# Kernel tuning notes

Measured on AMD Instinct MI355X. Metric: run time of the kernel, lower is better.

The kernel has to match this reference:

```python
import jax, jax.numpy as jnp
import numpy as np

L_LAYERS, D, H, FF_MUL = 4, 512, 8, 4
VOCAB, SEQ, MEM, CMEM, RATIO = 32000, 1024, 1024, 256, 4
DH = D // H


def _ln(x, g, b):
    mu = jnp.mean(x, -1, keepdims=True)
    var = jnp.mean((x - mu) ** 2, -1, keepdims=True)
    return (x - mu) / jnp.sqrt(var + 1e-5) * g + b


def _heads(x):
    b, n, _ = x.shape
    return x.reshape(b, n, H, -1).transpose(0, 2, 1, 3)  # [b,h,n,dh]


def _shift(x):
    # relative-position shift trick, x: [b,h,i,j] -> [b,h,i,j]
    b, h, i, j = x.shape
    x = jnp.concatenate([x, jnp.zeros((b, h, i, i), x.dtype)], -1)
    l = i + j - 1
    x = x.reshape(b, h, i * (i + j))
    pad = (-x.shape[-1]) % l
    x = jnp.pad(x, ((0, 0), (0, 0), (0, pad))).reshape(b, h, -1, l)
    return x[:, :, :i, i - 1:]


def _conv(x, w, b):
    # x: [B,L,D], w: [D_out, D_in, RATIO] (OIH), stride=RATIO
    y = jax.lax.conv_general_dilated(x.transpose(0, 2, 1), w, (RATIO,), 'VALID',
                                     dimension_numbers=('NCH', 'OIH', 'NCH'))
    return y.transpose(0, 2, 1) + b


def _full_attn(q, k, v):
    dots = jnp.einsum('bhid,bhjd->bhij', q, k) * (q.shape[-1] ** -0.5)
    return jnp.einsum('bhij,bhjd->bhid', jax.nn.softmax(dots, -1), v)


def setup_inputs() -> dict:
    key = jax.random.key(0)
    ks = jax.random.split(key, 24)
    s = 0.02
    return {
        'seq': jax.random.randint(ks[0], (4, SEQ), 0, VOCAB),
        'mask': jnp.ones((4, SEQ), dtype=bool),
        'mems': jax.random.normal(ks[1], (L_LAYERS, 4, MEM, D)) * s,
        'cmems': jax.random.normal(ks[2], (L_LAYERS, 4, CMEM, D)) * s,
        'pos_emb': jax.random.normal(ks[3], (H, CMEM + MEM + SEQ, DH)) * s,
        'embed': jax.random.normal(ks[4], (VOCAB, D)) * s,
        'ln1_g': jnp.ones((L_LAYERS, D)), 'ln1_b': jnp.zeros((L_LAYERS, D)),
        'Wq': jax.random.normal(ks[5], (L_LAYERS, D, D)) * s,
        'Wkv': jax.random.normal(ks[6], (L_LAYERS, D, 2 * D)) * s,
        'Wo': jax.random.normal(ks[7], (L_LAYERS, D, D)) * s,
        'bo': jnp.zeros((L_LAYERS, D)),
        'conv_w': jax.random.normal(ks[8], (L_LAYERS, D, D, RATIO)) * s,
        'conv_b': jnp.zeros((L_LAYERS, D)),
        'ln2_g': jnp.ones((L_LAYERS, D)), 'ln2_b': jnp.zeros((L_LAYERS, D)),
        'W1': jax.random.normal(ks[9], (L_LAYERS, D, FF_MUL * D)) * s,
        'b1': jnp.zeros((L_LAYERS, FF_MUL * D)),
        'W2': jax.random.normal(ks[10], (L_LAYERS, FF_MUL * D, D)) * s,
        'b2': jnp.zeros((L_LAYERS, D)),
    }


def _forward(seq, mask, mems, cmems, pos_emb, embed, ln1_g, ln1_b, Wq, Wkv, Wo, bo,
             conv_w, conv_b, ln2_g, ln2_b, W1, b1, W2, b2):
    scale = DH ** -0.5
    x = embed[seq]  # [b,t,d]
    maskb = mask.astype(bool)
    new_mems, new_cmems = [], []
    aux_total = jnp.zeros((), x.dtype)
    w_acc = 0.0
    for l in range(L_LAYERS):
        mem, cmem = mems[l], cmems[l]
        xn = _ln(x, ln1_g[l], ln1_b[l])
        q = _heads(xn @ Wq[l])
        kv_in = jnp.concatenate([cmem, mem, xn], 1)  # [b,kv_len,d]
        kv_len = kv_in.shape[1]
        k, v = jnp.split(kv_in @ Wkv[l], 2, -1)
        k, v = _heads(k), _heads(v)
        dots = jnp.einsum('bhid,bhjd->bhij', q, k) * scale
        pe = pos_emb[:, -kv_len:]
        dots = dots + _shift(jnp.einsum('bhid,hjd->bhij', q, pe) * scale)
        m2 = maskb[:, None, :, None] & maskb[:, None, None, :]  # [b,1,t,t]
        m2 = jnp.pad(m2, ((0, 0), (0, 0), (0, 0), (kv_len - SEQ, 0)), constant_values=True)
        dots = jnp.where(m2, dots, -jnp.finfo(dots.dtype).max)
        attn = jax.nn.softmax(dots, -1)
        w_acc = w_acc + jnp.mean(jax.lax.stop_gradient(attn), axis=(0, 1))
        out = jnp.einsum('bhij,bhjd->bhid', attn, v)
        out = out.transpose(0, 2, 1, 3).reshape(x.shape[0], SEQ, D)
        x = x + out @ Wo[l] + bo[l]
        # FIFO memory update (queue normed x, evict oldest)
        queue = jnp.concatenate([mem, xn], 1)
        old_mem, new_mem = queue[:, :-MEM], queue[:, -MEM:]
        pad_amt = old_mem.shape[1] % RATIO
        if pad_amt:
            old_mem = jnp.pad(old_mem, ((0, 0), (pad_amt, 0), (0, 0)))
        comp = _conv(old_mem, conv_w[l], conv_b[l])
        new_cmem = jnp.concatenate([cmem, comp], 1)[:, -CMEM:]
        new_mems.append(new_mem)
        new_cmems.append(new_cmem)
        # reconstruction (attention-reconstruction) aux loss
        old_mem_d = jax.lax.stop_gradient(old_mem)
        comp2 = _conv(old_mem_d, conv_w[l], conv_b[l])
        ck, cv = jnp.split(comp2 @ jax.lax.stop_gradient(Wkv[l]), 2, -1)
        ck, cv = _heads(ck), _heads(cv)
        start = kv_len - min(mem.shape[1], MEM) - SEQ
        ok = jax.lax.stop_gradient(k[:, :, start:kv_len - SEQ])
        ov = jax.lax.stop_gradient(v[:, :, start:kv_len - SEQ])
        qd = jax.lax.stop_gradient(q)
        aux_total = aux_total + jnp.mean((_full_attn(qd, ok, ov) - _full_attn(qd, ck, cv)) ** 2)
        # feed-forward block (PreNorm + Residual), exact GELU like torch nn.GELU
        xn2 = _ln(x, ln2_g[l], ln2_b[l])
        x = x + jax.nn.gelu(xn2 @ W1[l] + b1[l], approximate=False) @ W2[l] + b2[l]
    return (x, jnp.stack(new_mems), jnp.stack(new_cmems),
            aux_total / L_LAYERS, w_acc / L_LAYERS)


def reference(seq, mask, mems, cmems, pos_emb, embed, ln1_g, ln1_b, Wq, Wkv, Wo, bo,
              conv_w, conv_b, ln2_g, ln2_b, W1, b1, W2, b2):
    return _forward(seq, mask, mems, cmems, pos_emb, embed, ln1_g, ln1_b, Wq, Wkv, Wo, bo,
                    conv_w, conv_b, ln2_g, ln2_b, W1, b1, W2, b2)
```

## Files before the change

### kernel.cpp

```cpp
#include <hip/hip_runtime.h>
#include <hip/hip_bf16.h>


typedef __hip_bfloat16 bf16;
typedef short s16x8 __attribute__((ext_vector_type(8)));
typedef float f32x4 __attribute__((ext_vector_type(4)));

__device__ __forceinline__ f32x4 mfma16(s16x8 a, s16x8 b, f32x4 c) {
  return __builtin_amdgcn_mfma_f32_16x16x32_bf16(a, b, c, 0, 0, 0);
}

typedef __attribute__((address_space(1))) const void gvoid;
typedef __attribute__((address_space(3))) void lvoid;
__device__ __forceinline__ void gll16(const void* g, void* l) {
  __builtin_amdgcn_global_load_lds((gvoid*)g, (lvoid*)l, 16, 0, 0);
}

__device__ __forceinline__ float b2f(unsigned short u) {
  return __uint_as_float(((unsigned)u) << 16);
}
__device__ __forceinline__ unsigned short f2bb(float f) {
  bf16 h = __float2bfloat16(f);
  return *reinterpret_cast<unsigned short*>(&h);
}
__device__ __forceinline__ float ldf(const float* p) { return *p; }
__device__ __forceinline__ float ldf(const bf16* p) { return __bfloat162float(*p); }
__device__ __forceinline__ float4 ld4(const float* p) { return *(const float4*)p; }
__device__ __forceinline__ float4 ld4(const bf16* p) {
  const ushort4 u = *(const ushort4*)p;
  return make_float4(b2f(u.x), b2f(u.y), b2f(u.z), b2f(u.w));
}
__device__ __forceinline__ void st4(float* p, float4 r) { *(float4*)p = r; }
__device__ __forceinline__ void st4(bf16* p, float4 r) {
  *(ushort4*)p = make_ushort4(f2bb(r.x), f2bb(r.y), f2bb(r.z), f2bb(r.w));
}
__device__ __forceinline__ void stf(float* p, float v) { *p = v; }
__device__ __forceinline__ void stf(bf16* p, float v) { *p = __float2bfloat16(v); }

__global__ void probe_k(const void* ln1g, unsigned* flag) {
  if (threadIdx.x == 0) {
    const unsigned short u = *(const unsigned short*)ln1g;
    *flag = (u == 0x3F80u) ? 1u : 0u;
  }
}

template <int BM, int AMODE, bool ADD, bool BIAS, bool GELU, typename TC>
__global__ __launch_bounds__(256) void mgemm_k(
    const bf16* __restrict__ A, const int lda, const bf16* __restrict__ Bt,
    TC* __restrict__ C, const int ldc, const float* __restrict__ bias,
    const int K) {
  constexpr int NF = (BM == 128) ? 4 : 2;
  __shared__ bf16 As[BM * 64];
  __shared__ bf16 Bs[128 * 64];
  const int t = threadIdx.x, w = t >> 6, lane = t & 63;
  const int g = lane >> 4, li = lane & 15;
  const int m0 = blockIdx.y * BM, n0 = blockIdx.x << 7;
  const int wrow = (BM == 128) ? ((w >> 1) << 6) : 0;
  const int wcol = (BM == 128) ? ((w & 1) << 6) : (w << 5);
  f32x4 acc[4][NF];
#pragma unroll
  for (int mf = 0; mf < 4; mf++)
#pragma unroll
    for (int nf = 0; nf < NF; nf++)
#pragma unroll
      for (int e = 0; e < 4; e++) acc[mf][nf][e] = 0.f;
  constexpr int ACH = BM / 32;
  const int srow = lane >> 3, s8 = lane & 7;
  for (int k0 = 0; k0 < K; k0 += 64) {
    __syncthreads();
#pragma unroll
    for (int it = 0; it < ACH; it++) {
      const int chunk = w * ACH + it;
      const int row = (chunk << 3) + srow;
      const int k8 = s8 ^ (row & 7);
      const bf16* src;
      if constexpr (AMODE == 0) {
        src = A + (size_t)(m0 + row) * lda + k0 + (k8 << 3);
      } else if constexpr (AMODE == 1) {
        const int m = m0 + row;
        src = A + ((size_t)((m >> 8) * 2304 + 256) << 9) + (m & 255) * 2048 +
              k0 + (k8 << 3);
      } else {
        const int m = m0 + row;
        src = A + ((size_t)((m >> 10) * 2304 + 1280 + (m & 1023)) << 9) + k0 +
              (k8 << 3);
      }
      gll16(src, As + (chunk << 9));
    }
#pragma unroll
    for (int it = 0; it < 4; it++) {
      const int chunk = (w << 2) + it;
      const int row = (chunk << 3) + srow;
      const int k8 = s8 ^ (row & 7);
      gll16(Bt + (size_t)(n0 + row) * K + k0 + (k8 << 3), Bs + (chunk << 9));
    }
    __syncthreads();
#pragma unroll
    for (int ks = 0; ks < 2; ks++) {
      s16x8 af[4];
#pragma unroll
      for (int mf = 0; mf < 4; mf++) {
        const int row = wrow + (mf << 4) + li;
        af[mf] = *reinterpret_cast<const s16x8*>(
            As + (row << 6) + ((((ks << 2) + g) ^ (row & 7)) << 3));
      }
#pragma unroll
      for (int nf = 0; nf < NF; nf++) {
        const int col = wcol + (nf << 4) + li;
        const s16x8 bfr = *reinterpret_cast<const s16x8*>(
            Bs + (col << 6) + ((((ks << 2) + g) ^ (col & 7)) << 3));
#pragma unroll
        for (int mf = 0; mf < 4; mf++)
          acc[mf][nf] = mfma16(af[mf], bfr, acc[mf][nf]);
      }
    }
  }
#pragma unroll
  for (int mf = 0; mf < 4; mf++)
#pragma unroll
    for (int nf = 0; nf < NF; nf++) {
      const int n = n0 + wcol + (nf << 4) + li;
      const float bv = BIAS ? bias[n] : 0.f;
#pragma unroll
      for (int r = 0; r < 4; r++) {
        const int m = m0 + wrow + (mf << 4) + (g << 2) + r;
        float v = acc[mf][nf][r] + bv;
        if constexpr (GELU) v = 0.5f * v * (1.0f + erff(v * 0.70710678118f));
        TC* cp = C + (size_t)m * ldc + n;
        if constexpr (ADD)
          *cp += v;
        else
          stf(cp, v);
      }
    }
}

template <bool REL, bool DIFF, typename TO>
__global__ __launch_bounds__(256) void flash_k(
    const bf16* __restrict__ q, const bf16* __restrict__ kbase,
    const bf16* __restrict__ vbase, const int kvlen, const int ldkv,
    const int bstride, const bf16* __restrict__ pe, float2* __restrict__ ml,
    TO* __restrict__ outp, const float* __restrict__ prior,
    float* __restrict__ auxsum) {
  __shared__ short k_s[4096];
  __shared__ short v_s[4096];
  __shared__ short p_s[4096];
  __shared__ short pe_s[REL ? 8192 : 8];
  __shared__ float t_s[REL ? 5376 : 4];
  __shared__ float red_s[4];
  const int t = threadIdx.x, w = t >> 6, lane = t & 63;
  const int g = lane >> 4, li = lane & 15;
  const int i0 = blockIdx.x << 6, h = blockIdx.y, b = blockIdx.z;
  const bf16* qp =
      q + (size_t)(b * 1024 + i0 + (w << 4) + li) * 512 + (h << 6) + (g << 3);
  const s16x8 qf0 = *reinterpret_cast<const s16x8*>(qp);
  const s16x8 qf1 = *reinterpret_cast<const s16x8*>(qp + 32);
  const bf16* kpb = kbase + (size_t)b * bstride + (h << 6);
  const bf16* vpb = vbase + (size_t)b * bstride + (h << 6);
  const bf16* peh = REL ? pe + (size_t)h * 147456 : nullptr;
  float mreg[4] = {-1e30f, -1e30f, -1e30f, -1e30f};
  float lreg[4] = {0.f, 0.f, 0.f, 0.f};
  f32x4 o[4];
#pragma unroll
  for (int nt = 0; nt < 4; nt++)
#pragma unroll
    for (int e = 0; e < 4; e++) o[nt][e] = 0.f;

  for (int j0 = 0; j0 < kvlen; j0 += 64) {
    const int ub0 = j0 - i0 + 960;
    const bool doT = REL && (ub0 < 2304);
    __syncthreads();
    {
      const int r2 = t >> 3, c8 = t & 7;
#pragma unroll
      for (int it = 0; it < 2; it++) {
        const int row = (it << 5) + r2;
        const size_t gof = (size_t)(j0 + row) * ldkv + (c8 << 3);
        const s16x8 kk = *reinterpret_cast<const s16x8*>(kpb + gof);
        *reinterpret_cast<s16x8*>(
            k_s + (((row << 6) + (c8 << 3)) ^ ((row & 7) << 3))) = kk;
        const s16x8 vv = *reinterpret_cast<const s16x8*>(vpb + gof);
#pragma unroll
        for (int e = 0; e < 8; e++) {
          const int d = (c8 << 3) + e;
          v_s[((d << 6) + row) ^ (((c8 ^ e) & 7) << 3)] = vv[e];
        }
      }
      if (doT) {
#pragma unroll
        for (int it = 0; it < 4; it++) {
          const int idx = (it << 8) + t;
          const int row = idx >> 3, pc8 = idx & 7;
          const int u = ub0 + row;
          s16x8 pv = {0, 0, 0, 0, 0, 0, 0, 0};
          if (u < 2304)
            pv = *reinterpret_cast<const s16x8*>(peh + ((size_t)u << 6) + (pc8 << 3));
          *reinterpret_cast<s16x8*>(
              pe_s + (((row << 6) + (pc8 << 3)) ^ ((row & 7) << 3))) = pv;
        }
      }
    }
    __syncthreads();
    f32x4 s[4];
#pragma unroll
    for (int nt = 0; nt < 4; nt++) {
#pragma unroll
      for (int e = 0; e < 4; e++) s[nt][e] = 0.f;
      const int rb = (((nt << 4) + li) << 6) + (g << 3);
      const int sw = (li & 7) << 3;
      const s16x8 kb0 = *reinterpret_cast<const s16x8*>(k_s + (rb ^ sw));
      const s16x8 kb1 = *reinterpret_cast<const s16x8*>(k_s + ((rb + 32) ^ sw));
      s[nt] = mfma16(qf0, kb0, s[nt]);
      s[nt] = mfma16(qf1, kb1, s[nt]);
    }
    if (doT) {
      float* tw = t_s + w * 1344;
      const int urb = 48 - (w << 4);
#pragma unroll
      for (int ut = 0; ut < 5; ut++) {
        f32x4 tt;
#pragma unroll
        for (int e = 0; e < 4; e++) tt[e] = 0.f;
        const int prb = ((urb + (ut << 4) + li) << 6) + (g << 3);
        const int sw = (li & 7) << 3;
        const s16x8 pb0 = *reinterpret_cast<const s16x8*>(pe_s + (prb ^ sw));
        const s16x8 pb1 = *reinterpret_cast<const s16x8*>(pe_s + ((prb + 32) ^ sw));
        tt = mfma16(qf0, pb0, tt);
        tt = mfma16(qf1, pb1, tt);
#pragma unroll
        for (int r = 0; r < 4; r++) tw[((g << 2) + r) * 84 + (ut << 4) + li] = tt[r];
      }
#pragma unroll
      for (int nt = 0; nt < 4; nt++)
#pragma unroll
        for (int r = 0; r < 4; r++)
          s[nt][r] += tw[((g << 2) + r) * 83 + (nt << 4) + li + 15];
    }
#pragma unroll
    for (int nt = 0; nt < 4; nt++)
#pragma unroll
      for (int e = 0; e < 4; e++) s[nt][e] *= 0.125f;
    float pr[4][4];
#pragma unroll
    for (int r = 0; r < 4; r++) {
      float tm = fmaxf(fmaxf(s[0][r], s[1][r]), fmaxf(s[2][r], s[3][r]));
#pragma unroll
      for (int off = 1; off < 16; off <<= 1) tm = fmaxf(tm, __shfl_xor(tm, off));
      const float mn = fmaxf(mreg[r], tm);
      const float al = __expf(mreg[r] - mn);
      mreg[r] = mn;
      float te = 0.f;
#pragma unroll
      for (int nt = 0; nt < 4; nt++) {
        pr[nt][r] = __expf(s[nt][r] - mn);
        te += pr[nt][r];
      }
#pragma unroll
      for (int off = 1; off < 16; off <<= 1) te += __shfl_xor(te, off);
      lreg[r] = lreg[r] * al + te;
#pragma unroll
      for (int nt = 0; nt < 4; nt++) o[nt][r] *= al;
    }
    short* pw = p_s + (w << 10);
#pragma unroll
    for (int nt = 0; nt < 4; nt++)
#pragma unroll
      for (int r = 0; r < 4; r++) {
        const int il = (g << 2) + r;
        pw[((il << 6) + (nt << 4) + li) ^ ((il & 7) << 3)] = (short)f2bb(pr[nt][r]);
      }
#pragma unroll
    for (int ks = 0; ks < 2; ks++) {
      const s16x8 pa = *reinterpret_cast<const s16x8*>(
          pw + (((li << 6) + (ks << 5) + (g << 3)) ^ ((li & 7) << 3)));
#pragma unroll
      for (int nt = 0; nt < 4; nt++) {
        const int d = (nt << 4) + li;
        const s16x8 vb = *reinterpret_cast<const s16x8*>(
            v_s + (((d << 6) + (ks << 5) + (g << 3)) ^ ((((d >> 3) ^ (d & 7)) & 7) << 3)));
        o[nt] = mfma16(pa, vb, o[nt]);
      }
    }
  }
  float rl[4];
#pragma unroll
  for (int r = 0; r < 4; r++) rl[r] = 1.0f / lreg[r];
  if constexpr (REL) {
    if (li == 0) {
#pragma unroll
      for (int r = 0; r < 4; r++)
        ml[(size_t)((b << 3) + h) * 1024 + i0 + (w << 4) + (g << 2) + r] =
            make_float2(mreg[r], lreg[r]);
    }
  }
  if constexpr (!DIFF) {
#pragma unroll
    for (int nt = 0; nt < 4; nt++)
#pragma unroll
      for (int r = 0; r < 4; r++) {
        const size_t adr = (size_t)(b * 1024 + i0 + (w << 4) + (g << 2) + r) * 512 +
                           (h << 6) + (nt << 4) + li;
        stf(outp + adr, o[nt][r] * rl[r]);
      }
  } else {
    float sq = 0.f;
#pragma unroll
    for (int nt = 0; nt < 4; nt++)
#pragma unroll
      for (int r = 0; r < 4; r++) {
        const size_t adr = (size_t)(b * 1024 + i0 + (w << 4) + (g << 2) + r) * 512 +
                           (h << 6) + (nt << 4) + li;
        const float dv = o[nt][r] * rl[r] - prior[adr];
        sq = fmaf(dv, dv, sq);
      }
#pragma unroll
    for (int off = 1; off < 64; off <<= 1) sq += __shfl_xor(sq, off);
    if (lane == 0) red_s[w] = sq;
    __syncthreads();
    if (t == 0) atomicAdd(auxsum, red_s[0] + red_s[1] + red_s[2] + red_s[3]);
  }
}

__global__ __launch_bounds__(256) void wacc_k(const bf16* __restrict__ q,
                                              const bf16* __restrict__ kv,
                                              const bf16* __restrict__ pe,
                                              const float2* __restrict__ ml,
                                              float* __restrict__ w_acc) {
  __shared__ short k_s[4096];
  __shared__ short pe_s[8192];
  __shared__ float t_s[5376];
  __shared__ float2 ml_s[64];
  const int t = threadIdx.x, w = t >> 6, lane = t & 63;
  const int g = lane >> 4, li = lane & 15;
  const int i0 = blockIdx.x << 6, j0 = blockIdx.y << 6;
  const int ub0 = j0 - i0 + 960;
  const bool doT = (ub0 < 2304);
  f32x4 acc[4];
#pragma unroll
  for (int nt = 0; nt < 4; nt++)
#pragma unroll
    for (int e = 0; e < 4; e++) acc[nt][e] = 0.f;
  for (int h = 0; h < 8; h++) {
    __syncthreads();
    if (doT) {
      const bf16* peh = pe + (size_t)h * 147456;
#pragma unroll
      for (int it = 0; it < 4; it++) {
        const int idx = (it << 8) + t;
        const int row = idx >> 3, pc8 = idx & 7;
        const int u = ub0 + row;
        s16x8 pv = {0, 0, 0, 0, 0, 0, 0, 0};
        if (u < 2304)
          pv = *reinterpret_cast<const s16x8*>(peh + ((size_t)u << 6) + (pc8 << 3));
        *reinterpret_cast<s16x8*>(
            pe_s + (((row << 6) + (pc8 << 3)) ^ ((row & 7) << 3))) = pv;
      }
    }
    for (int b = 0; b < 4; b++) {
      __syncthreads();
      {
        const int r2 = t >> 3, c8 = t & 7;
        const bf16* kpb = kv + (size_t)b * 2359296 + (h << 6);
#pragma unroll
        for (int it = 0; it < 2; it++) {
          const int row = (it << 5) + r2;
          const s16x8 kk = *reinterpret_cast<const s16x8*>(
              kpb + (size_t)(j0 + row) * 1024 + (c8 << 3));
          *reinterpret_cast<s16x8*>(
              k_s + (((row << 6) + (c8 << 3)) ^ ((row & 7) << 3))) = kk;
        }
        if (t < 64) {
          float2 v = ml[(size_t)((b << 3) + h) * 1024 + i0 + t];
          v.y = 1.0f / v.y;
          ml_s[t] = v;
        }
      }
      __syncthreads();
      const bf16* qp =
          q + (size_t)(b * 1024 + i0 + (w << 4) + li) * 512 + (h << 6) + (g << 3);
      const s16x8 qf0 = *reinterpret_cast<const s16x8*>(qp);
      const s16x8 qf1 = *reinterpret_cast<const s16x8*>(qp + 32);
      f32x4 s[4];
#pragma unroll
      for (int nt = 0; nt < 4; nt++) {
#pragma unroll
        for (int e = 0; e < 4; e++) s[nt][e] = 0.f;
        const int rb = (((nt << 4) + li) << 6) + (g << 3);
        const int sw = (li & 7) << 3;
        const s16x8 kb0 = *reinterpret_cast<const s16x8*>(k_s + (rb ^ sw));
        const s16x8 kb1 = *reinterpret_cast<const s16x8*>(k_s + ((rb + 32) ^ sw));
        s[nt] = mfma16(qf0, kb0, s[nt]);
        s[nt] = mfma16(qf1, kb1, s[nt]);
      }
      if (doT) {
        float* tw = t_s + w * 1344;
        const int urb = 48 - (w << 4);
#pragma unroll
        for (int ut = 0; ut < 5; ut++) {
          f32x4 tt;
#pragma unroll
          for (int e = 0; e < 4; e++) tt[e] = 0.f;
          const int prb = ((urb + (ut << 4) + li) << 6) + (g << 3);
          const int sw = (li & 7) << 3;
          const s16x8 pb0 = *reinterpret_cast<const s16x8*>(pe_s + (prb ^ sw));
          const s16x8 pb1 = *reinterpret_cast<const s16x8*>(pe_s + ((prb + 32) ^ sw));
          tt = mfma16(qf0, pb0, tt);
          tt = mfma16(qf1, pb1, tt);
#pragma unroll
          for (int r = 0; r < 4; r++)
            tw[((g << 2) + r) * 84 + (ut << 4) + li] = tt[r];
        }
#pragma unroll
        for (int nt = 0; nt < 4; nt++)
#pragma unroll
          for (int r = 0; r < 4; r++)
            s[nt][r] += tw[((g << 2) + r) * 83 + (nt << 4) + li + 15];
      }
#pragma unroll
      for (int nt = 0; nt < 4; nt++)
#pragma unroll
        for (int r = 0; r < 4; r++) {
          const float sv = s[nt][r] * 0.125f;
          const float2 st = ml_s[(w << 4) + (g << 2) + r];
          acc[nt][r] += __expf(sv - st.x) * st.y;
        }
    }
  }
#pragma unroll
  for (int nt = 0; nt < 4; nt++)
#pragma unroll
    for (int r = 0; r < 4; r++) {
      float* wp = w_acc + (size_t)(i0 + (w << 4) + (g << 2) + r) * 2304 + j0 +
                  (nt << 4) + li;
      *wp += acc[nt][r];
    }
}

template <typename TIN>
__global__ __launch_bounds__(256) void wtr_k(
    const TIN* __restrict__ Wq, const TIN* __restrict__ Wkv,
    const TIN* __restrict__ Wo, const TIN* __restrict__ W1,
    const TIN* __restrict__ W2, bf16* __restrict__ WT,
    const unsigned* flag, unsigned want) {
  if (*flag != want) return;
  __shared__ bf16 tile[64][65];
  int bx = blockIdx.x;
  const TIN* W;
  bf16* dst;
  int N, K;
  if (bx < 64) {
    W = Wq; dst = WT; N = 512; K = 512;
  } else if (bx < 192) {
    W = Wkv; dst = WT + 262144; N = 1024; K = 512; bx -= 64;
  } else if (bx < 256) {
    W = Wo; dst = WT + 786432; N = 512; K = 512; bx -= 192;
  } else if (bx < 512) {
    W = W1; dst = WT + 1048576; N = 2048; K = 512; bx -= 256;
  } else {
    W = W2; dst = WT + 2097152; N = 512; K = 2048; bx -= 512;
  }
  const int tn = N >> 6;
  const int kt = bx / tn, nt = bx - kt * tn;
  const int k0 = kt << 6, n0 = nt << 6;
  const int t = threadIdx.x;
#pragma unroll
  for (int i = 0; i < 16; i++) {
    const int idx = (i << 8) + t;
    const int kr = idx >> 6, nc = idx & 63;
    tile[kr][nc] = __float2bfloat16(ldf(W + (size_t)(k0 + kr) * N + n0 + nc));
  }
  __syncthreads();
#pragma unroll
  for (int i = 0; i < 16; i++) {
    const int idx = (i << 8) + t;
    const int nr = idx >> 6, kc = idx & 63;
    dst[(size_t)(n0 + nr) * K + k0 + kc] = tile[kc][nr];
  }
}

template <typename TIN>
__global__ void wcp_k(const TIN* __restrict__ cw, bf16* __restrict__ WcT,
                      const unsigned* flag, unsigned want) {
  if (*flag != want) return;
  const int id = blockIdx.x * 256 + threadIdx.x;
  const int o = id >> 11, p = id & 2047;
  const int r = p >> 9, i = p & 511;
  WcT[id] = __float2bfloat16(ldf(cw + ((size_t)o << 11) + (i << 2) + r));
}

template <typename TIN>
__global__ void kvb_k(const TIN* __restrict__ cmem, const TIN* __restrict__ mem,
                      bf16* __restrict__ kvin, const unsigned* flag, unsigned want) {
  if (*flag != want) return;
  const int id = blockIdx.x * 256 + threadIdx.x;
  const int row = id >> 7, c4 = (id & 127) << 2;
  const int b = row / 1280, j = row - b * 1280;
  const TIN* src = (j < 256) ? cmem + (((size_t)(b * 256 + j)) << 9) + c4
                             : mem + (((size_t)(b * 1024 + j - 256)) << 9) + c4;
  st4(kvin + (((size_t)(b * 2304 + j)) << 9) + c4, ld4(src));
}

template <typename TIN>
__global__ void bcvt_k(const TIN* __restrict__ bo, const TIN* __restrict__ cb,
                       const TIN* __restrict__ b1, const TIN* __restrict__ b2,
                       float* __restrict__ bws, const unsigned* flag, unsigned want) {
  if (*flag != want) return;
  const int id = blockIdx.x * 256 + threadIdx.x;
  const int l = id / 3584, r = id - l * 3584;
  float v;
  if (r < 512) v = ldf(bo + l * 512 + r);
  else if (r < 1024) v = ldf(cb + l * 512 + r - 512);
  else if (r < 3072) v = ldf(b1 + l * 2048 + r - 1024);
  else v = ldf(b2 + l * 512 + r - 3072);
  bws[id] = v;
}

template <typename TIN, typename TY>
__global__ __launch_bounds__(256) void ln_k(const float* __restrict__ x,
                                            const TIN* __restrict__ g,
                                            const TIN* __restrict__ bta,
                                            TY* __restrict__ y, bf16* kvx,
                                            const unsigned* flag, unsigned want) {
  if (*flag != want) return;
  const int w = threadIdx.x >> 6, lane = threadIdx.x & 63;
  const size_t row = (size_t)blockIdx.x * 4 + w;
  const float* xr = x + row * 512;
  float v[8], s = 0, ss = 0;
#pragma unroll
  for (int i = 0; i < 8; i++) {
    v[i] = xr[lane + (i << 6)];
    s += v[i];
    ss = fmaf(v[i], v[i], ss);
  }
#pragma unroll
  for (int off = 1; off < 64; off <<= 1) {
    s += __shfl_xor(s, off);
    ss += __shfl_xor(ss, off);
  }
  const float mu = s * (1.0f / 512.0f);
  const float var = ss * (1.0f / 512.0f) - mu * mu;
  const float inv = rsqrtf(var + 1e-5f);
  bf16* k2 = kvx ? kvx + (((row >> 10) * 2304 + 1280 + (row & 1023)) << 9) : nullptr;
#pragma unroll
  for (int i = 0; i < 8; i++) {
    const int c = lane + (i << 6);
    const float val = (v[i] - mu) * inv * ldf(g + c) + ldf(bta + c);
    stf(y + row * 512 + c, val);
    if (k2) k2[c] = __float2bfloat16(val);
  }
}

template <typename TIN>
__global__ void embed_k(const int* __restrict__ seq, const TIN* __restrict__ emb,
                        float* __restrict__ x, const unsigned* flag, unsigned want) {
  if (*flag != want) return;
  const int row = blockIdx.x;
  const int tok = seq[row];
  const TIN* e = emb + (size_t)tok * 512;
  float* xr = x + (size_t)row * 512;
  for (int c = threadIdx.x; c < 512; c += 256) xr[c] = ldf(e + c);
}

template <typename TIN>
__global__ void cvtpe_k(const TIN* __restrict__ pe, bf16* __restrict__ peb,
                        const unsigned* flag, unsigned want) {
  if (*flag != want) return;
  const int i = blockIdx.x * 256 + threadIdx.x;
  peb[i] = __float2bfloat16(ldf(pe + i));
}

__global__ void zero_k(float* __restrict__ p, int n) {
  for (int i = blockIdx.x * 256 + threadIdx.x; i < n; i += gridDim.x * 256) p[i] = 0.0f;
}

template <typename TOUT>
__global__ void cpy_k(const bf16* __restrict__ s, TOUT* __restrict__ d, int n,
                      const unsigned* flag, unsigned want) {
  if (*flag != want) return;
  for (int i = blockIdx.x * 256 + threadIdx.x; i < n; i += gridDim.x * 256)
    stf(d + i, ldf(s + i));
}

template <typename TOUT>
__global__ void f2bs_k(const float* __restrict__ s, TOUT* __restrict__ d, float sc,
                       int n, const unsigned* flag, unsigned want) {
  if (*flag != want) return;
  for (int i = blockIdx.x * 256 + threadIdx.x; i < n; i += gridDim.x * 256)
    stf(d + i, s[i] * sc);
}

template <typename TOUT>
__global__ void fin_aux_k(const float* __restrict__ acc, TOUT* __restrict__ d,
                          const unsigned* flag, unsigned want) {
  if (*flag != want) return;
  if (threadIdx.x == 0) stf(d, acc[0] * (1.0f / 8388608.0f));
}

extern "C" void kernel_launch(void* const* d_in, const int* in_sizes, int n_in,
                              void* d_out, int out_size, void* d_ws, size_t ws_size,
                              hipStream_t stream) {
  typedef const bf16 CB;
  typedef const float CF;
  const int* seq = (const int*)d_in[0];
  CB *mems_b = (CB*)d_in[2], *cmems_b = (CB*)d_in[3], *pe_b = (CB*)d_in[4],
     *emb_b = (CB*)d_in[5], *l1g_b = (CB*)d_in[6], *l1b_b = (CB*)d_in[7],
     *Wq_b = (CB*)d_in[8], *Wkv_b = (CB*)d_in[9], *Wo_b = (CB*)d_in[10],
     *bo_b = (CB*)d_in[11], *cw_b = (CB*)d_in[12], *cb_b = (CB*)d_in[13],
     *l2g_b = (CB*)d_in[14], *l2b_b = (CB*)d_in[15], *W1_b = (CB*)d_in[16],
     *b1_b = (CB*)d_in[17], *W2_b = (CB*)d_in[18], *b2_b = (CB*)d_in[19];
  CF *mems_f = (CF*)d_in[2], *cmems_f = (CF*)d_in[3], *pe_f = (CF*)d_in[4],
     *emb_f = (CF*)d_in[5], *l1g_f = (CF*)d_in[6], *l1b_f = (CF*)d_in[7],
     *Wq_f = (CF*)d_in[8], *Wkv_f = (CF*)d_in[9], *Wo_f = (CF*)d_in[10],
     *bo_f = (CF*)d_in[11], *cw_f = (CF*)d_in[12], *cb_f = (CF*)d_in[13],
     *l2g_f = (CF*)d_in[14], *l2b_f = (CF*)d_in[15], *W1_f = (CF*)d_in[16],
     *b1_f = (CF*)d_in[17], *W2_f = (CF*)d_in[18], *b2_f = (CF*)d_in[19];
  bf16* outb = (bf16*)d_out;
  float* outf = (float*)d_out;

  float* ws = (float*)d_ws;
  float* x = ws;
  bf16* q = (bf16*)(ws + 2097152);
  bf16* kv = (bf16*)(ws + 3145728);
  bf16* mid = (bf16*)(ws + 3145728);
  float* region = ws + 7864320;
  bf16* attn_o = (bf16*)region;
  float* aux1 = region;
  bf16* xn2 = (bf16*)region;
  bf16* ckcv = (bf16*)(ws + 9961472);
  float* w_acc = ws + 10485760;
  bf16* cmp_ws = (bf16*)(ws + 12845056);
  float2* ml = (float2*)(ws + 13369344);
  float* auxsum = ws + 13434880;
  unsigned* flag = (unsigned*)(ws + 13434881);
  bf16* pe_w = (bf16*)(ws + 13434884);
  float* bias_ws = ws + 14024708;
  bf16* kvin = (bf16*)(ws + 14039044);
  bf16* WT = (bf16*)(ws + 16398340);

  probe_k<<<1, 64, 0, stream>>>(d_in[6], flag);
  zero_k<<<2048, 256, 0, stream>>>(w_acc, 2359296);
  zero_k<<<1, 256, 0, stream>>>(auxsum, 1);
  embed_k<bf16><<<4096, 256, 0, stream>>>(seq, emb_b, x, flag, 1);
  embed_k<float><<<4096, 256, 0, stream>>>(seq, emb_f, x, flag, 0);
  cvtpe_k<bf16><<<4608, 256, 0, stream>>>(pe_b, pe_w, flag, 1);
  cvtpe_k<float><<<4608, 256, 0, stream>>>(pe_f, pe_w, flag, 0);
  bcvt_k<bf16><<<56, 256, 0, stream>>>(bo_b, cb_b, b1_b, b2_b, bias_ws, flag, 1);
  bcvt_k<float><<<56, 256, 0, stream>>>(bo_f, cb_f, b1_f, b2_f, bias_ws, flag, 0);

  for (int l = 0; l < 4; l++) {
    bf16* xnl_b = outb + 2097152 + (size_t)l * 2097152;
    float* xnl_f = outf + 2097152 + (size_t)l * 2097152;
    bf16* cmp_b = outb + 10485760 + (size_t)l * 524288;
    float* cmp_f = outf + 10485760 + (size_t)l * 524288;
    const float* bl = bias_ws + l * 3584;

    wtr_k<bf16><<<768, 256, 0, stream>>>(Wq_b + (size_t)l * 262144,
        Wkv_b + (size_t)l * 524288, Wo_b + (size_t)l * 262144,
        W1_b + (size_t)l * 1048576, W2_b + (size_t)l * 1048576, WT, flag, 1);
    wtr_k<float><<<768, 256, 0, stream>>>(Wq_f + (size_t)l * 262144,
        Wkv_f + (size_t)l * 524288, Wo_f + (size_t)l * 262144,
        W1_f + (size_t)l * 1048576, W2_f + (size_t)l * 1048576, WT, flag, 0);
    wcp_k<bf16><<<4096, 256, 0, stream>>>(cw_b + (size_t)l * 1048576, WT + 3145728, flag, 1);
    wcp_k<float><<<4096, 256, 0, stream>>>(cw_f + (size_t)l * 1048576, WT + 3145728, flag, 0);
    kvb_k<bf16><<<2560, 256, 0, stream>>>(cmems_b + (size_t)l * 524288,
                                          mems_b + (size_t)l * 2097152, kvin, flag, 1);
    kvb_k<float><<<2560, 256, 0, stream>>>(cmems_f + (size_t)l * 524288,
                                           mems_f + (size_t)l * 2097152, kvin, flag, 0);
    ln_k<bf16, bf16><<<1024, 256, 0, stream>>>(x, l1g_b + l * 512, l1b_b + l * 512,
                                               xnl_b, kvin, flag, 1);
    ln_k<float, float><<<1024, 256, 0, stream>>>(x, l1g_f + l * 512, l1b_f + l * 512,
                                                 xnl_f, kvin, flag, 0);
    mgemm_k<64, 2, false, false, false, bf16><<<dim3(4, 64), 256, 0, stream>>>(
        kvin, 512, WT, q, 512, nullptr, 512);
    mgemm_k<128, 0, false, false, false, bf16><<<dim3(8, 72), 256, 0, stream>>>(
        kvin, 512, WT + 262144, kv, 1024, nullptr, 512);
    flash_k<true, false, bf16><<<dim3(16, 8, 4), 256, 0, stream>>>(
        q, kv, kv + 512, 2304, 1024, 2359296, pe_w, ml, attn_o, nullptr, nullptr);
    wacc_k<<<dim3(16, 36), 256, 0, stream>>>(q, kv, pe_w, ml, w_acc);
    mgemm_k<64, 0, true, true, false, float><<<dim3(4, 64), 256, 0, stream>>>(
        attn_o, 512, WT + 786432, x, 512, bl, 512);
    mgemm_k<64, 1, false, true, false, bf16><<<dim3(4, 16), 256, 0, stream>>>(
        kvin, 0, WT + 3145728, cmp_ws, 512, bl + 512, 2048);
    cpy_k<bf16><<<512, 256, 0, stream>>>(cmp_ws, cmp_b, 524288, flag, 1);
    cpy_k<float><<<512, 256, 0, stream>>>(cmp_ws, cmp_f, 524288, flag, 0);
    mgemm_k<64, 0, false, false, false, bf16><<<dim3(8, 16), 256, 0, stream>>>(
        cmp_ws, 512, WT + 262144, ckcv, 1024, nullptr, 512);
    flash_k<false, false, float><<<dim3(16, 8, 4), 256, 0, stream>>>(
        q, kv + 262144, kv + 262144 + 512, 1024, 1024, 2359296, nullptr, nullptr,
        aux1, nullptr, nullptr);
    flash_k<false, true, float><<<dim3(16, 8, 4), 256, 0, stream>>>(
        q, ckcv, ckcv + 512, 256, 1024, 262144, nullptr, nullptr,
        (float*)nullptr, aux1, auxsum);
    ln_k<bf16, bf16><<<1024, 256, 0, stream>>>(x, l2g_b + l * 512, l2b_b + l * 512,
                                               xn2, nullptr, flag, 1);
    ln_k<float, bf16><<<1024, 256, 0, stream>>>(x, l2g_f + l * 512, l2b_f + l * 512,
                                                xn2, nullptr, flag, 0);
    mgemm_k<128, 0, false, true, true, bf16><<<dim3(16, 32), 256, 0, stream>>>(
        xn2, 512, WT + 1048576, mid, 2048, bl + 1024, 512);
    mgemm_k<64, 0, true, true, false, float><<<dim3(4, 64), 256, 0, stream>>>(
        mid, 2048, WT + 2097152, x, 512, bl + 3072, 2048);
  }

  f2bs_k<bf16><<<2048, 256, 0, stream>>>(x, outb, 1.0f, 2097152, flag, 1);
  f2bs_k<float><<<2048, 256, 0, stream>>>(x, outf, 1.0f, 2097152, flag, 0);
  f2bs_k<bf16><<<2048, 256, 0, stream>>>(w_acc, outb + 12582913, 1.0f / 128.0f, 2359296, flag, 1);
  f2bs_k<float><<<2048, 256, 0, stream>>>(w_acc, outf + 12582913, 1.0f / 128.0f, 2359296, flag, 0);
  fin_aux_k<bf16><<<1, 64, 0, stream>>>(auxsum, outb + 12582912, flag, 1);
  fin_aux_k<float><<<1, 64, 0, stream>>>(auxsum, outf + 12582912, flag, 0);
}
```

Baseline: 2.031 ms.

## Split flash attention KV range across blocks with merge; shuffle-based rel-pos shift

Attention over the KV sequence is split into two halves handled by separate blocks. Each block writes unnormalized partial outputs and its max/sum stats, and a new merge kernel combines them. The aim is more blocks per launch for the 512-block grids, better occupancy on the many CUs. The relative-position shift now uses register shuffles instead of an LDS staging buffer, which frees shared memory and enables launch_bounds of 4. The w_acc kernel is also split over head groups using atomicAdd. In exchange this adds extra fp32 partial-output traffic, a merge launch, and atomic contention.

```diff
diff --git a/kernel.cpp b/kernel.cpp
--- a/kernel.cpp
+++ b/kernel.cpp
@@ -135,8 +135,8 @@
     }
 }
 
-template <bool REL, bool DIFF, typename TO>
-__global__ __launch_bounds__(256) void flash_k(
+template <bool REL, bool DIFF, int NS, typename TO>
+__global__ __launch_bounds__(256, 4) void flash_k(
     const bf16* __restrict__ q, const bf16* __restrict__ kbase,
     const bf16* __restrict__ vbase, const int kvlen, const int ldkv,
     const int bstride, const bf16* __restrict__ pe, float2* __restrict__ ml,
@@ -146,11 +146,12 @@
   __shared__ short v_s[4096];
   __shared__ short p_s[4096];
   __shared__ short pe_s[REL ? 8192 : 8];
-  __shared__ float t_s[REL ? 5376 : 4];
-  __shared__ float red_s[4];
   const int t = threadIdx.x, w = t >> 6, lane = t & 63;
   const int g = lane >> 4, li = lane & 15;
-  const int i0 = blockIdx.x << 6, h = blockIdx.y, b = blockIdx.z;
+  const int i0 = blockIdx.x << 4 << 2, h = blockIdx.y;
+  const int b = blockIdx.z / NS, sp = blockIdx.z % NS;
+  const int span = kvlen / NS;
+  const int jlo = sp * span, jhi = jlo + span;
   const bf16* qp =
       q + (size_t)(b * 1024 + i0 + (w << 4) + li) * 512 + (h << 6) + (g << 3);
   const s16x8 qf0 = *reinterpret_cast<const s16x8*>(qp);
@@ -166,7 +167,7 @@
 #pragma unroll
     for (int e = 0; e < 4; e++) o[nt][e] = 0.f;
 
-  for (int j0 = 0; j0 < kvlen; j0 += 64) {
+  for (int j0 = jlo; j0 < jhi; j0 += 64) {
     const int ub0 = j0 - i0 + 960;
     const bool doT = REL && (ub0 < 2304);
     __syncthreads();
@@ -213,28 +214,35 @@
       s[nt] = mfma16(qf0, kb0, s[nt]);
       s[nt] = mfma16(qf1, kb1, s[nt]);
     }
-    if (doT) {
-      float* tw = t_s + w * 1344;
-      const int urb = 48 - (w << 4);
-#pragma unroll
-      for (int ut = 0; ut < 5; ut++) {
-        f32x4 tt;
-#pragma unroll
-        for (int e = 0; e < 4; e++) tt[e] = 0.f;
-        const int prb = ((urb + (ut << 4) + li) << 6) + (g << 3);
-        const int sw = (li & 7) << 3;
-        const s16x8 pb0 = *reinterpret_cast<const s16x8*>(pe_s + (prb ^ sw));
-        const s16x8 pb1 = *reinterpret_cast<const s16x8*>(pe_s + ((prb + 32) ^ sw));
-        tt = mfma16(qf0, pb0, tt);
-        tt = mfma16(qf1, pb1, tt);
-#pragma unroll
-        for (int r = 0; r < 4; r++) tw[((g << 2) + r) * 84 + (ut << 4) + li] = tt[r];
-      }
-#pragma unroll
-      for (int nt = 0; nt < 4; nt++)
-#pragma unroll
-        for (int r = 0; r < 4; r++)
-          s[nt][r] += tw[((g << 2) + r) * 83 + (nt << 4) + li + 15];
+    if constexpr (REL) {
+      if (doT) {
+        f32x4 t5[5];
+        const int urb = 48 - (w << 4);
+#pragma unroll
+        for (int ut = 0; ut < 5; ut++) {
+#pragma unroll
+          for (int e = 0; e < 4; e++) t5[ut][e] = 0.f;
+          const int prb = ((urb + (ut << 4) + li) << 6) + (g << 3);
+          const int sw = (li & 7) << 3;
+          const s16x8 pb0 = *reinterpret_cast<const s16x8*>(pe_s + (prb ^ sw));
+          const s16x8 pb1 = *reinterpret_cast<const s16x8*>(pe_s + ((prb + 32) ^ sw));
+          t5[ut] = mfma16(qf0, pb0, t5[ut]);
+          t5[ut] = mfma16(qf1, pb1, t5[ut]);
+        }
+#pragma unroll
+        for (int r = 0; r < 4; r++) {
+          const int il = (g << 2) + r;
+          const int local = li - il + 15;
+          const int srcl = (g << 4) | (local & 15);
+          float tv[5];
+#pragma unroll
+          for (int ut = 0; ut < 5; ut++) tv[ut] = __shfl(t5[ut][r], srcl);
+          const bool hi = local >= 16;
+#pragma unroll
+          for (int nt = 0; nt < 4; nt++)
+            s[nt][r] += hi ? tv[nt + 1] : tv[nt];
+        }
+      }
     }
 #pragma unroll
     for (int nt = 0; nt < 4; nt++)
@@ -282,42 +290,82 @@
       }
     }
   }
-  float rl[4];
-#pragma unroll
-  for (int r = 0; r < 4; r++) rl[r] = 1.0f / lreg[r];
-  if constexpr (REL) {
+  if constexpr (NS > 1) {
     if (li == 0) {
 #pragma unroll
       for (int r = 0; r < 4; r++)
-        ml[(size_t)((b << 3) + h) * 1024 + i0 + (w << 4) + (g << 2) + r] =
+        ml[(size_t)((sp << 5) + (b << 3) + h) * 1024 + i0 + (w << 4) + (g << 2) + r] =
             make_float2(mreg[r], lreg[r]);
     }
-  }
-  if constexpr (!DIFF) {
 #pragma unroll
     for (int nt = 0; nt < 4; nt++)
 #pragma unroll
       for (int r = 0; r < 4; r++) {
-        const size_t adr = (size_t)(b * 1024 + i0 + (w << 4) + (g << 2) + r) * 512 +
-                           (h << 6) + (nt << 4) + li;
-        stf(outp + adr, o[nt][r] * rl[r]);
+        const size_t adr =
+            (size_t)((sp * 4 + b) * 1024 + i0 + (w << 4) + (g << 2) + r) * 512 +
+            (h << 6) + (nt << 4) + li;
+        outp[adr] = o[nt][r];
       }
   } else {
-    float sq = 0.f;
-#pragma unroll
-    for (int nt = 0; nt < 4; nt++)
-#pragma unroll
-      for (int r = 0; r < 4; r++) {
-        const size_t adr = (size_t)(b * 1024 + i0 + (w << 4) + (g << 2) + r) * 512 +
-                           (h << 6) + (nt << 4) + li;
-        const float dv = o[nt][r] * rl[r] - prior[adr];
-        sq = fmaf(dv, dv, sq);
-      }
-#pragma unroll
-    for (int off = 1; off < 64; off <<= 1) sq += __shfl_xor(sq, off);
-    if (lane == 0) red_s[w] = sq;
-    __syncthreads();
-    if (t == 0) atomicAdd(auxsum, red_s[0] + red_s[1] + red_s[2] + red_s[3]);
+    float rl[4];
+#pragma unroll
+    for (int r = 0; r < 4; r++) rl[r] = 1.0f / lreg[r];
+    if constexpr (!DIFF) {
+#pragma unroll
+      for (int nt = 0; nt < 4; nt++)
+#pragma unroll
+        for (int r = 0; r < 4; r++) {
+          const size_t adr = (size_t)(b * 1024 + i0 + (w << 4) + (g << 2) + r) * 512 +
+                             (h << 6) + (nt << 4) + li;
+          stf(outp + adr, o[nt][r] * rl[r]);
+        }
+    } else {
+      float sq = 0.f;
+#pragma unroll
+      for (int nt = 0; nt < 4; nt++)
+#pragma unroll
+        for (int r = 0; r < 4; r++) {
+          const size_t adr = (size_t)(b * 1024 + i0 + (w << 4) + (g << 2) + r) * 512 +
+                             (h << 6) + (nt << 4) + li;
+          const float dv = o[nt][r] * rl[r] - prior[adr];
+          sq = fmaf(dv, dv, sq);
+        }
+#pragma unroll
+      for (int off = 1; off < 64; off <<= 1) sq += __shfl_xor(sq, off);
+      float* fl = reinterpret_cast<float*>(p_s);
+      __syncthreads();
+      if (lane == 0) fl[w] = sq;
+      __syncthreads();
+      if (t == 0) atomicAdd(auxsum, fl[0] + fl[1] + fl[2] + fl[3]);
+    }
+  }
+}
+
+template <typename TOUT, bool MLOUT>
+__global__ __launch_bounds__(256) void merge_k(const float* __restrict__ o_part,
+                                               const float2* __restrict__ mlp,
+                                               TOUT* __restrict__ out,
+                                               float2* __restrict__ mlf) {
+  const int id = blockIdx.x * 256 + threadIdx.x;
+  const int row = id >> 7, c4 = (id & 127) << 2;
+  const int b = row >> 10, i = row & 1023, h = c4 >> 6;
+  const size_t mlrow = (size_t)((b << 3) + h) * 1024 + i;
+  const float2 s1 = mlp[mlrow];
+  const float2 s2 = mlp[32768 + mlrow];
+  const float m = fmaxf(s1.x, s2.x);
+  const float w1 = __expf(s1.x - m), w2 = __expf(s2.x - m);
+  const float l = w1 * s1.y + w2 * s2.y;
+  const float rl = 1.0f / l;
+  const float4 a = *(const float4*)(o_part + (size_t)row * 512 + c4);
+  const float4 bq = *(const float4*)(o_part + 2097152 + (size_t)row * 512 + c4);
+  float4 r;
+  r.x = (w1 * a.x + w2 * bq.x) * rl;
+  r.y = (w1 * a.y + w2 * bq.y) * rl;
+  r.z = (w1 * a.z + w2 * bq.z) * rl;
+  r.w = (w1 * a.w + w2 * bq.w) * rl;
+  st4(out + (size_t)row * 512 + c4, r);
+  if constexpr (MLOUT) {
+    if ((c4 & 63) == 0) mlf[mlrow] = make_float2(m, l);
   }
 }
 
@@ -328,11 +376,11 @@
                                               float* __restrict__ w_acc) {
   __shared__ short k_s[4096];
   __shared__ short pe_s[8192];
-  __shared__ float t_s[5376];
   __shared__ float2 ml_s[64];
   const int t = threadIdx.x, w = t >> 6, lane = t & 63;
   const int g = lane >> 4, li = lane & 15;
   const int i0 = blockIdx.x << 6, j0 = blockIdx.y << 6;
+  const int h0 = blockIdx.z << 2;
   const int ub0 = j0 - i0 + 960;
   const bool doT = (ub0 < 2304);
   f32x4 acc[4];
@@ -340,7 +388,8 @@
   for (int nt = 0; nt < 4; nt++)
 #pragma unroll
     for (int e = 0; e < 4; e++) acc[nt][e] = 0.f;
-  for (int h = 0; h < 8; h++) {
+  for (int hh = 0; hh < 4; hh++) {
+    const int h = h0 + hh;
     __syncthreads();
     if (doT) {
       const bf16* peh = pe + (size_t)h * 147456;
@@ -393,28 +442,32 @@
         s[nt] = mfma16(qf1, kb1, s[nt]);
       }
       if (doT) {
-        float* tw = t_s + w * 1344;
+        f32x4 t5[5];
         const int urb = 48 - (w << 4);
 #pragma unroll
         for (int ut = 0; ut < 5; ut++) {
-          f32x4 tt;
-#pragma unroll
-          for (int e = 0; e < 4; e++) tt[e] = 0.f;
+#pragma unroll
+          for (int e = 0; e < 4; e++) t5[ut][e] = 0.f;
           const int prb = ((urb + (ut << 4) + li) << 6) + (g << 3);
           const int sw = (li & 7) << 3;
           const s16x8 pb0 = *reinterpret_cast<const s16x8*>(pe_s + (prb ^ sw));
           const s16x8 pb1 = *reinterpret_cast<const s16x8*>(pe_s + ((prb + 32) ^ sw));
-          tt = mfma16(qf0, pb0, tt);
-          tt = mfma16(qf1, pb1, tt);
-#pragma unroll
-          for (int r = 0; r < 4; r++)
-            tw[((g << 2) + r) * 84 + (ut << 4) + li] = tt[r];
-        }
-#pragma unroll
-        for (int nt = 0; nt < 4; nt++)
-#pragma unroll
-          for (int r = 0; r < 4; r++)
-            s[nt][r] += tw[((g << 2) + r) * 83 + (nt << 4) + li + 15];
+          t5[ut] = mfma16(qf0, pb0, t5[ut]);
+          t5[ut] = mfma16(qf1, pb1, t5[ut]);
+        }
+#pragma unroll
+        for (int r = 0; r < 4; r++) {
+          const int il = (g << 2) + r;
+          const int local = li - il + 15;
+          const int srcl = (g << 4) | (local & 15);
+          float tv[5];
+#pragma unroll
+          for (int ut = 0; ut < 5; ut++) tv[ut] = __shfl(t5[ut][r], srcl);
+          const bool hi = local >= 16;
+#pragma unroll
+          for (int nt = 0; nt < 4; nt++)
+            s[nt][r] += hi ? tv[nt + 1] : tv[nt];
+        }
       }
 #pragma unroll
       for (int nt = 0; nt < 4; nt++)
@@ -432,7 +485,7 @@
     for (int r = 0; r < 4; r++) {
       float* wp = w_acc + (size_t)(i0 + (w << 4) + (g << 2) + r) * 2304 + j0 +
                   (nt << 4) + li;
-      *wp += acc[nt][r];
+      atomicAdd(wp, acc[nt][r]);
     }
 }
 
@@ -636,6 +689,8 @@
   float* bias_ws = ws + 14024708;
   bf16* kvin = (bf16*)(ws + 14039044);
   bf16* WT = (bf16*)(ws + 16398340);
+  float* o_part = ws + 18757636;
+  float2* ml_part = (float2*)(ws + 22951940);
 
   probe_k<<<1, 64, 0, stream>>>(d_in[6], flag);
   zero_k<<<2048, 256, 0, stream>>>(w_acc, 2359296);
@@ -674,9 +729,10 @@
         kvin, 512, WT, q, 512, nullptr, 512);
     mgemm_k<128, 0, false, false, false, bf16><<<dim3(8, 72), 256, 0, stream>>>(
         kvin, 512, WT + 262144, kv, 1024, nullptr, 512);
-    flash_k<true, false, bf16><<<dim3(16, 8, 4), 256, 0, stream>>>(
-        q, kv, kv + 512, 2304, 1024, 2359296, pe_w, ml, attn_o, nullptr, nullptr);
-    wacc_k<<<dim3(16, 36), 256, 0, stream>>>(q, kv, pe_w, ml, w_acc);
+    flash_k<true, false, 2, float><<<dim3(16, 8, 8), 256, 0, stream>>>(
+        q, kv, kv + 512, 2304, 1024, 2359296, pe_w, ml_part, o_part, nullptr, nullptr);
+    merge_k<bf16, true><<<2048, 256, 0, stream>>>(o_part, ml_part, attn_o, ml);
+    wacc_k<<<dim3(16, 36, 2), 256, 0, stream>>>(q, kv, pe_w, ml, w_acc);
     mgemm_k<64, 0, true, true, false, float><<<dim3(4, 64), 256, 0, stream>>>(
         attn_o, 512, WT + 786432, x, 512, bl, 512);
     mgemm_k<64, 1, false, true, false, bf16><<<dim3(4, 16), 256, 0, stream>>>(
@@ -685,10 +741,11 @@
     cpy_k<float><<<512, 256, 0, stream>>>(cmp_ws, cmp_f, 524288, flag, 0);
     mgemm_k<64, 0, false, false, false, bf16><<<dim3(8, 16), 256, 0, stream>>>(
         cmp_ws, 512, WT + 262144, ckcv, 1024, nullptr, 512);
-    flash_k<false, false, float><<<dim3(16, 8, 4), 256, 0, stream>>>(
-        q, kv + 262144, kv + 262144 + 512, 1024, 1024, 2359296, nullptr, nullptr,
-        aux1, nullptr, nullptr);
-    flash_k<false, true, float><<<dim3(16, 8, 4), 256, 0, stream>>>(
+    flash_k<false, false, 2, float><<<dim3(16, 8, 8), 256, 0, stream>>>(
+        q, kv + 262144, kv + 262144 + 512, 1024, 1024, 2359296, nullptr, ml_part,
+        o_part, nullptr, nullptr);
+    merge_k<float, false><<<2048, 256, 0, stream>>>(o_part, ml_part, aux1, nullptr);
+    flash_k<false, true, 1, float><<<dim3(16, 8, 4), 256, 0, stream>>>(
         q, ckcv, ckcv + 512, 256, 1024, 262144, nullptr, nullptr,
         (float*)nullptr, aux1, auxsum);
     ln_k<bf16, bf16><<<1024, 256, 0, stream>>>(x, l2g_b + l * 512, l2b_b + l * 512,
```

Result: slower. 2.407 ms (+18.6%).
